# Performance work log

Measured on AMD Instinct MI355X. Metric: run time of the kernel, lower is better.

The kernel has to match this reference:

```python
import jax, jax.numpy as jnp
import numpy as np

B, C, H, W = 32, 256, 64, 64
EPS = 1e-8  # clamp for cosine-similarity denominators


def setup_inputs() -> dict:
    key = jax.random.key(0)
    k1, k2, k3 = jax.random.split(key, 3)
    unmasked = jax.random.normal(k1, (B, C, H, W), dtype=jnp.float32)
    masked = jax.random.normal(k2, (B, C, H, W), dtype=jnp.float32)
    latent_mask = jax.random.randint(k3, (B, H, W), 0, 2, dtype=jnp.int32)
    return {
        "unmasked_latent_tensors": unmasked,
        "masked_latent_tensors": masked,
        "latent_mask": latent_mask,
    }


def reference(unmasked_latent_tensors, masked_latent_tensors, latent_mask):
    # Original torch code builds a full [B, B*H*W, H, W] cross-activation of a
    # cosine-similarity 1x1 conv (input vs. every masked position used as a
    # prototype), then gathers only the diagonal entries where batch index and
    # spatial position match. Mathematically that diagonal is just the
    # per-position cosine similarity along the channel axis, computed here
    # directly.
    u = unmasked_latent_tensors
    m = masked_latent_tensors
    num = jnp.sum(u * m, axis=1)                       # [B, H, W]
    u_norm = jnp.sqrt(jnp.sum(u * u, axis=1))          # [B, H, W]
    m_norm = jnp.sqrt(jnp.sum(m * m, axis=1))          # [B, H, W]
    sim = num / (jnp.maximum(u_norm, EPS) * jnp.maximum(m_norm, EPS))
    # masked=True: average similarity over mask==1 positions.
    mask_f = (latent_mask != 0).astype(sim.dtype)      # [B, H, W]
    return jnp.sum(sim * mask_f) / jnp.sum(mask_f)
```

## Files before the change

kernel.cpp:

```cpp
#include <hip/hip_runtime.h>


#define BB   32
#define CC   256
#define HH   64
#define WW   64
#define HWSZ (HH * WW)
#define NPOS (BB * HWSZ)
#define HW4  (HWSZ / 4)
#define PPB  256
#define NW   16
#define CPW  (CC / NW)
#define NBLK (NPOS / PPB)
#define SIM_EPS 1e-8f

__global__ __launch_bounds__(1024) void
sim_reduce_kernel(const float4* __restrict__ u4,
                  const float4* __restrict__ m4,
                  const int*    __restrict__ mask,
                  double*       __restrict__ ws,
                  float*        __restrict__ out)
{
    __shared__ float4 s_num[NW][64];
    __shared__ float4 s_uu [NW][64];
    __shared__ float4 s_mm [NW][64];

    const int wv = threadIdx.x >> 6;
    const int l  = threadIdx.x & 63;

    const int pos0 = blockIdx.x * PPB;
    const int b    = pos0 >> 12;
    const int hw0  = pos0 & (HWSZ - 1);

    int mk = 0;
    if (threadIdx.x < PPB) mk = mask[pos0 + threadIdx.x];

    const size_t base4 = (size_t)b * CC * HW4
                       + (size_t)(wv * CPW) * HW4
                       + (size_t)(hw0 >> 2) + (size_t)l;
    const float4* __restrict__ up = u4 + base4;
    const float4* __restrict__ mp = m4 + base4;

    float4 num = make_float4(0.f, 0.f, 0.f, 0.f);
    float4 uu  = make_float4(0.f, 0.f, 0.f, 0.f);
    float4 mm  = make_float4(0.f, 0.f, 0.f, 0.f);

#pragma unroll 4
    for (int c = 0; c < CPW; ++c) {
        const float4 a  = up[(size_t)c * HW4];
        const float4 bv = mp[(size_t)c * HW4];
        num.x = fmaf(a.x, bv.x, num.x);
        num.y = fmaf(a.y, bv.y, num.y);
        num.z = fmaf(a.z, bv.z, num.z);
        num.w = fmaf(a.w, bv.w, num.w);
        uu.x  = fmaf(a.x, a.x,  uu.x);
        uu.y  = fmaf(a.y, a.y,  uu.y);
        uu.z  = fmaf(a.z, a.z,  uu.z);
        uu.w  = fmaf(a.w, a.w,  uu.w);
        mm.x  = fmaf(bv.x, bv.x, mm.x);
        mm.y  = fmaf(bv.y, bv.y, mm.y);
        mm.z  = fmaf(bv.z, bv.z, mm.z);
        mm.w  = fmaf(bv.w, bv.w, mm.w);
    }

    s_num[wv][l] = num;
    s_uu [wv][l] = uu;
    s_mm [wv][l] = mm;
    __syncthreads();

    double sd = 0.0, md = 0.0;
    if (threadIdx.x < PPB) {
        const int t = threadIdx.x;
        float fn = 0.f, fu = 0.f, fm = 0.f;
#pragma unroll
        for (int k = 0; k < NW; ++k) {
            fn += ((const float*)s_num[k])[t];
            fu += ((const float*)s_uu [k])[t];
            fm += ((const float*)s_mm [k])[t];
        }
        const float denom = fmaxf(sqrtf(fu), SIM_EPS) * fmaxf(sqrtf(fm), SIM_EPS);
        const float sim   = fn / denom;
        if (mk != 0) { sd = (double)sim; md = 1.0; }
    }

#pragma unroll
    for (int off = 32; off > 0; off >>= 1) {
        sd += __shfl_down(sd, off, 64);
        md += __shfl_down(md, off, 64);
    }

    __shared__ double r_s[NW];
    __shared__ double r_m[NW];
    if (l == 0) { r_s[wv] = sd; r_m[wv] = md; }
    __syncthreads();

    if (threadIdx.x == 0) {
        double ts = 0.0, tm = 0.0;
#pragma unroll
        for (int k = 0; k < NW; ++k) { ts += r_s[k]; tm += r_m[k]; }
        atomicAdd(&ws[0], ts);
        atomicAdd(&ws[1], tm);
        __threadfence();
        const unsigned long long prev =
            atomicAdd((unsigned long long*)&ws[2], 1ull);
        if (prev == (unsigned long long)(NBLK - 1)) {
            const double s  = atomicAdd(&ws[0], 0.0);
            const double mc = atomicAdd(&ws[1], 0.0);
            out[0] = (float)(s / mc);
        }
    }
}

extern "C" void kernel_launch(void* const* d_in, const int* in_sizes, int n_in,
                              void* d_out, int out_size, void* d_ws, size_t ws_size,
                              hipStream_t stream)
{
    const float4* u4   = (const float4*)d_in[0];
    const float4* m4   = (const float4*)d_in[1];
    const int*    mask = (const int*)d_in[2];
    float*  out = (float*)d_out;
    double* ws  = (double*)d_ws;

    hipMemsetAsync(d_ws, 0, 3 * sizeof(double), stream);

    sim_reduce_kernel<<<NBLK, 1024, 0, stream>>>(u4, m4, mask, ws, out);
}
```

Measured before the change: 296.6 us.

## Split cosine-similarity reduction into channel-chunk partial and combine kernels

New measurement: 294.0 us. Within noise of the previous version (-0.9%).

```diff
diff --git a/kernel.cpp b/kernel.cpp
--- a/kernel.cpp
+++ b/kernel.cpp
@@ -1,109 +1,205 @@
 #include <hip/hip_runtime.h>
 
 
-#define BB   32
-#define CC   256
-#define HH   64
-#define WW   64
-#define HWSZ (HH * WW)
-#define NPOS (BB * HWSZ)
-#define HW4  (HWSZ / 4)
-#define PPB  256
-#define NW   16
-#define CPW  (CC / NW)
-#define NBLK (NPOS / PPB)
+#define BB    32
+#define CC    256
+#define HWSZ  4096
+#define NPOS  (BB * HWSZ)
+#define HW4   (HWSZ / 4)
+#define NP4   (NPOS / 4)
+#define CHUNK 16
+#define NCH   (CC / CHUNK)
+#define NBLK_A (BB * NCH)
+#define THR_A  512
+#define THR_B  512
+#define NBLK_B (NP4 / THR_B)
 #define SIM_EPS 1e-8f
 
-__global__ __launch_bounds__(1024) void
-sim_reduce_kernel(const float4* __restrict__ u4,
-                  const float4* __restrict__ m4,
-                  const int*    __restrict__ mask,
-                  double*       __restrict__ ws,
-                  float*        __restrict__ out)
-{
-    __shared__ float4 s_num[NW][64];
-    __shared__ float4 s_uu [NW][64];
-    __shared__ float4 s_mm [NW][64];
-
+#define WS_PART_F4 (NCH * 3 * NP4)
+#define WS_NEED    ((size_t)WS_PART_F4 * 16 + 64)
+
+__global__ __launch_bounds__(THR_A) void
+partial_kernel(const float4* __restrict__ u4,
+               const float4* __restrict__ m4,
+               float4* __restrict__ wsp)
+{
+    const int blk = blockIdx.x;
+    const int b   = blk >> 4;
+    const int ch  = blk & (NCH - 1);
+    const int tid = threadIdx.x;
+
+    const size_t base4 = ((size_t)b * CC + (size_t)ch * CHUNK) * HW4;
+    const float4* __restrict__ up = u4 + base4 + tid;
+    const float4* __restrict__ mp = m4 + base4 + tid;
+
+    float4 n0 = make_float4(0.f,0.f,0.f,0.f), n1 = n0;
+    float4 s0 = n0, s1 = n0;
+    float4 t0 = n0, t1 = n0;
+
+#pragma unroll 2
+    for (int cc = 0; cc < CHUNK; ++cc) {
+        const size_t o = (size_t)cc * HW4;
+        const float4 a0 = up[o];
+        const float4 b0 = mp[o];
+        const float4 a1 = up[o + 512];
+        const float4 b1 = mp[o + 512];
+
+        n0.x = fmaf(a0.x, b0.x, n0.x); n0.y = fmaf(a0.y, b0.y, n0.y);
+        n0.z = fmaf(a0.z, b0.z, n0.z); n0.w = fmaf(a0.w, b0.w, n0.w);
+        s0.x = fmaf(a0.x, a0.x, s0.x); s0.y = fmaf(a0.y, a0.y, s0.y);
+        s0.z = fmaf(a0.z, a0.z, s0.z); s0.w = fmaf(a0.w, a0.w, s0.w);
+        t0.x = fmaf(b0.x, b0.x, t0.x); t0.y = fmaf(b0.y, b0.y, t0.y);
+        t0.z = fmaf(b0.z, b0.z, t0.z); t0.w = fmaf(b0.w, b0.w, t0.w);
+
+        n1.x = fmaf(a1.x, b1.x, n1.x); n1.y = fmaf(a1.y, b1.y, n1.y);
+        n1.z = fmaf(a1.z, b1.z, n1.z); n1.w = fmaf(a1.w, b1.w, n1.w);
+        s1.x = fmaf(a1.x, a1.x, s1.x); s1.y = fmaf(a1.y, a1.y, s1.y);
+        s1.z = fmaf(a1.z, a1.z, s1.z); s1.w = fmaf(a1.w, a1.w, s1.w);
+        t1.x = fmaf(b1.x, b1.x, t1.x); t1.y = fmaf(b1.y, b1.y, t1.y);
+        t1.z = fmaf(b1.z, b1.z, t1.z); t1.w = fmaf(b1.w, b1.w, t1.w);
+    }
+
+    const int p0 = b * HW4 + tid;
+    const int p1 = p0 + 512;
+    wsp[(ch * 3 + 0) * NP4 + p0] = n0;
+    wsp[(ch * 3 + 1) * NP4 + p0] = s0;
+    wsp[(ch * 3 + 2) * NP4 + p0] = t0;
+    wsp[(ch * 3 + 0) * NP4 + p1] = n1;
+    wsp[(ch * 3 + 1) * NP4 + p1] = s1;
+    wsp[(ch * 3 + 2) * NP4 + p1] = t1;
+}
+
+__global__ __launch_bounds__(THR_B) void
+combine_kernel(const float4* __restrict__ wsp,
+               const int4*   __restrict__ mask4,
+               double*       __restrict__ tail,
+               float*        __restrict__ out)
+{
+    const int p4 = blockIdx.x * THR_B + threadIdx.x;
+
+    float4 fn = make_float4(0.f,0.f,0.f,0.f);
+    float4 fu = fn, fm = fn;
+#pragma unroll 4
+    for (int ch = 0; ch < NCH; ++ch) {
+        const float4 a = wsp[(ch * 3 + 0) * NP4 + p4];
+        const float4 b = wsp[(ch * 3 + 1) * NP4 + p4];
+        const float4 c = wsp[(ch * 3 + 2) * NP4 + p4];
+        fn.x += a.x; fn.y += a.y; fn.z += a.z; fn.w += a.w;
+        fu.x += b.x; fu.y += b.y; fu.z += b.z; fu.w += b.w;
+        fm.x += c.x; fm.y += c.y; fm.z += c.z; fm.w += c.w;
+    }
+
+    const int4 mk = mask4[p4];
+    double sd = 0.0, md = 0.0;
+    {
+        const float d0 = fmaxf(sqrtf(fu.x), SIM_EPS) * fmaxf(sqrtf(fm.x), SIM_EPS);
+        const float d1 = fmaxf(sqrtf(fu.y), SIM_EPS) * fmaxf(sqrtf(fm.y), SIM_EPS);
+        const float d2 = fmaxf(sqrtf(fu.z), SIM_EPS) * fmaxf(sqrtf(fm.z), SIM_EPS);
+        const float d3 = fmaxf(sqrtf(fu.w), SIM_EPS) * fmaxf(sqrtf(fm.w), SIM_EPS);
+        if (mk.x != 0) { sd += (double)(fn.x / d0); md += 1.0; }
+        if (mk.y != 0) { sd += (double)(fn.y / d1); md += 1.0; }
+        if (mk.z != 0) { sd += (double)(fn.z / d2); md += 1.0; }
+        if (mk.w != 0) { sd += (double)(fn.w / d3); md += 1.0; }
+    }
+
+#pragma unroll
+    for (int off = 32; off > 0; off >>= 1) {
+        sd += __shfl_down(sd, off, 64);
+        md += __shfl_down(md, off, 64);
+    }
+
+    __shared__ double rs[THR_B / 64];
+    __shared__ double rm[THR_B / 64];
     const int wv = threadIdx.x >> 6;
     const int l  = threadIdx.x & 63;
-
-    const int pos0 = blockIdx.x * PPB;
+    if (l == 0) { rs[wv] = sd; rm[wv] = md; }
+    __syncthreads();
+
+    if (threadIdx.x == 0) {
+        double ts = 0.0, tm = 0.0;
+#pragma unroll
+        for (int k = 0; k < THR_B / 64; ++k) { ts += rs[k]; tm += rm[k]; }
+        atomicAdd(&tail[0], ts);
+        atomicAdd(&tail[1], tm);
+        __threadfence();
+        const unsigned long long prev =
+            atomicAdd((unsigned long long*)&tail[2], 1ull);
+        if (prev == (unsigned long long)(NBLK_B - 1)) {
+            const double s  = atomicAdd(&tail[0], 0.0);
+            const double mc = atomicAdd(&tail[1], 0.0);
+            out[0] = (float)(s / mc);
+        }
+    }
+}
+
+__global__ __launch_bounds__(512) void
+fallback_kernel(const float4* __restrict__ u4,
+                const float4* __restrict__ m4,
+                const int*    __restrict__ mask,
+                double*       __restrict__ ws,
+                float*        __restrict__ out)
+{
+    __shared__ float4 s_num[8][64];
+    __shared__ float4 s_uu [8][64];
+    __shared__ float4 s_mm [8][64];
+
+    const int wv = threadIdx.x >> 6;
+    const int l  = threadIdx.x & 63;
+    const int pos0 = blockIdx.x * 256;
     const int b    = pos0 >> 12;
     const int hw0  = pos0 & (HWSZ - 1);
 
-    int mk = 0;
-    if (threadIdx.x < PPB) mk = mask[pos0 + threadIdx.x];
-
-    const size_t base4 = (size_t)b * CC * HW4
-                       + (size_t)(wv * CPW) * HW4
+    const size_t base4 = (size_t)b * CC * HW4 + (size_t)(wv * 32) * HW4
                        + (size_t)(hw0 >> 2) + (size_t)l;
     const float4* __restrict__ up = u4 + base4;
     const float4* __restrict__ mp = m4 + base4;
 
-    float4 num = make_float4(0.f, 0.f, 0.f, 0.f);
-    float4 uu  = make_float4(0.f, 0.f, 0.f, 0.f);
-    float4 mm  = make_float4(0.f, 0.f, 0.f, 0.f);
-
+    float4 num = make_float4(0.f,0.f,0.f,0.f), uu = num, mm = num;
 #pragma unroll 4
-    for (int c = 0; c < CPW; ++c) {
+    for (int c = 0; c < 32; ++c) {
         const float4 a  = up[(size_t)c * HW4];
         const float4 bv = mp[(size_t)c * HW4];
-        num.x = fmaf(a.x, bv.x, num.x);
-        num.y = fmaf(a.y, bv.y, num.y);
-        num.z = fmaf(a.z, bv.z, num.z);
-        num.w = fmaf(a.w, bv.w, num.w);
-        uu.x  = fmaf(a.x, a.x,  uu.x);
-        uu.y  = fmaf(a.y, a.y,  uu.y);
-        uu.z  = fmaf(a.z, a.z,  uu.z);
-        uu.w  = fmaf(a.w, a.w,  uu.w);
-        mm.x  = fmaf(bv.x, bv.x, mm.x);
-        mm.y  = fmaf(bv.y, bv.y, mm.y);
-        mm.z  = fmaf(bv.z, bv.z, mm.z);
-        mm.w  = fmaf(bv.w, bv.w, mm.w);
-    }
-
-    s_num[wv][l] = num;
-    s_uu [wv][l] = uu;
-    s_mm [wv][l] = mm;
+        num.x = fmaf(a.x, bv.x, num.x); num.y = fmaf(a.y, bv.y, num.y);
+        num.z = fmaf(a.z, bv.z, num.z); num.w = fmaf(a.w, bv.w, num.w);
+        uu.x  = fmaf(a.x, a.x, uu.x);   uu.y  = fmaf(a.y, a.y, uu.y);
+        uu.z  = fmaf(a.z, a.z, uu.z);   uu.w  = fmaf(a.w, a.w, uu.w);
+        mm.x  = fmaf(bv.x, bv.x, mm.x); mm.y  = fmaf(bv.y, bv.y, mm.y);
+        mm.z  = fmaf(bv.z, bv.z, mm.z); mm.w  = fmaf(bv.w, bv.w, mm.w);
+    }
+    s_num[wv][l] = num; s_uu[wv][l] = uu; s_mm[wv][l] = mm;
     __syncthreads();
 
     double sd = 0.0, md = 0.0;
-    if (threadIdx.x < PPB) {
+    if (threadIdx.x < 256) {
         const int t = threadIdx.x;
         float fn = 0.f, fu = 0.f, fm = 0.f;
 #pragma unroll
-        for (int k = 0; k < NW; ++k) {
+        for (int k = 0; k < 8; ++k) {
             fn += ((const float*)s_num[k])[t];
             fu += ((const float*)s_uu [k])[t];
             fm += ((const float*)s_mm [k])[t];
         }
         const float denom = fmaxf(sqrtf(fu), SIM_EPS) * fmaxf(sqrtf(fm), SIM_EPS);
-        const float sim   = fn / denom;
-        if (mk != 0) { sd = (double)sim; md = 1.0; }
-    }
-
+        if (mask[pos0 + t] != 0) { sd = (double)(fn / denom); md = 1.0; }
+    }
 #pragma unroll
     for (int off = 32; off > 0; off >>= 1) {
         sd += __shfl_down(sd, off, 64);
         md += __shfl_down(md, off, 64);
     }
-
-    __shared__ double r_s[NW];
-    __shared__ double r_m[NW];
-    if (l == 0) { r_s[wv] = sd; r_m[wv] = md; }
+    __shared__ double rs[8], rm[8];
+    if (l == 0) { rs[wv] = sd; rm[wv] = md; }
     __syncthreads();
-
     if (threadIdx.x == 0) {
         double ts = 0.0, tm = 0.0;
 #pragma unroll
-        for (int k = 0; k < NW; ++k) { ts += r_s[k]; tm += r_m[k]; }
+        for (int k = 0; k < 8; ++k) { ts += rs[k]; tm += rm[k]; }
         atomicAdd(&ws[0], ts);
         atomicAdd(&ws[1], tm);
         __threadfence();
         const unsigned long long prev =
             atomicAdd((unsigned long long*)&ws[2], 1ull);
-        if (prev == (unsigned long long)(NBLK - 1)) {
+        if (prev == (unsigned long long)((NPOS / 256) - 1)) {
             const double s  = atomicAdd(&ws[0], 0.0);
             const double mc = atomicAdd(&ws[1], 0.0);
             out[0] = (float)(s / mc);
@@ -118,10 +214,17 @@
     const float4* u4   = (const float4*)d_in[0];
     const float4* m4   = (const float4*)d_in[1];
     const int*    mask = (const int*)d_in[2];
-    float*  out = (float*)d_out;
-    double* ws  = (double*)d_ws;
-
-    hipMemsetAsync(d_ws, 0, 3 * sizeof(double), stream);
-
-    sim_reduce_kernel<<<NBLK, 1024, 0, stream>>>(u4, m4, mask, ws, out);
-}
+    float* out = (float*)d_out;
+
+    if (ws_size >= WS_NEED) {
+        double* tail = (double*)((char*)d_ws + (size_t)WS_PART_F4 * 16);
+        hipMemsetAsync(tail, 0, 64, stream);
+        partial_kernel<<<NBLK_A, THR_A, 0, stream>>>(u4, m4, (float4*)d_ws);
+        combine_kernel<<<NBLK_B, THR_B, 0, stream>>>((const float4*)d_ws,
+                                                     (const int4*)mask, tail, out);
+    } else {
+        hipMemsetAsync(d_ws, 0, 3 * sizeof(double), stream);
+        fallback_kernel<<<NPOS / 256, 512, 0, stream>>>(u4, m4, mask,
+                                                        (double*)d_ws, out);
+    }
+}
```
